# Optimization experiments

Hardware: AMD Instinct MI355X
Metric: run time of the kernel (lower is better)

Reference implementation:

```python
import math
import jax, jax.numpy as jnp
import numpy as np

B, CIN, H, W = 1, 64, 56, 56
MID, HEADS, COUT, MPOS = 32, 8, 64, 56


def setup_inputs() -> dict:
    key = jax.random.key(0)
    ks = jax.random.split(key, 11)
    s = 0.05
    return {
        "x": jax.random.normal(ks[0], (B, CIN, H, W), jnp.float32),
        "Wq": jax.random.normal(ks[1], (MID * HEADS, CIN), jnp.float32) * s,
        "bq": jax.random.normal(ks[2], (MID * HEADS,), jnp.float32) * s,
        "Wk": jax.random.normal(ks[3], (MID * HEADS, CIN), jnp.float32) * s,
        "bk": jax.random.normal(ks[4], (MID * HEADS,), jnp.float32) * s,
        "Wv": jax.random.normal(ks[5], (MID * HEADS, CIN), jnp.float32) * s,
        "bv": jax.random.normal(ks[6], (MID * HEADS,), jnp.float32) * s,
        "Wo": jax.random.normal(ks[7], (COUT, MID * HEADS), jnp.float32) * s,
        "bo": jax.random.normal(ks[8], (COUT,), jnp.float32) * s,
        "row_emb_table": jax.random.normal(ks[9], (2 * MPOS - 1, MID // 2), jnp.float32) * s,
        "col_emb_table": jax.random.normal(ks[10], (2 * MPOS - 1, MID // 2), jnp.float32) * s,
    }


def _conv1x1(x, Wt, bt):
    # 1x1 Conv2d == channel-wise linear
    return jnp.einsum('bcij,dc->bdij', x, Wt) + bt[None, :, None, None]


def reference(x, Wq, bq, Wk, bk, Wv, bv, Wo, bo, row_emb_table, col_emb_table):
    b, cin, h, w = x.shape
    inv = 1.0 / math.sqrt(cin)
    q = _conv1x1(x, Wq, bq).reshape(b, MID, HEADS, h, w)
    k = _conv1x1(x, Wk, bk).reshape(b, MID, HEADS, h, w)
    # relative position indices (constant, derived from arange)
    rel = (jnp.arange(MPOS)[None, :] - jnp.arange(MPOS)[:, None]) + MPOS - 1
    row_emb = row_emb_table[rel[:w, :w].reshape(-1)].T.reshape(MID // 2, w, w)
    col_emb = col_emb_table[rel[:h, :h].reshape(-1)].T.reshape(MID // 2, h, h)
    q_row, q_col = q[:, :MID // 2], q[:, MID // 2:]
    row_scores = jnp.einsum('bchij,cik->bhijk', q_row, row_emb)  # [b,H,h,w,h]
    col_scores = jnp.einsum('bchij,cjl->bhijl', q_col, col_emb)  # [b,H,h,w,w]
    scores = (row_scores[..., :, None] + col_scores[..., None, :]) * inv
    scores = scores + jnp.einsum('bchij,bchkl->bhijkl', q, k) * inv  # [b,H,h,w,h,w]
    probs = jax.nn.softmax(scores.reshape(b, HEADS, h, w, -1), axis=-1).reshape(scores.shape)
    v = _conv1x1(x, Wv, bv).reshape(b, MID, HEADS, h, w)
    o = jnp.einsum('bhijkl,bchkl->bchij', probs, v)
    out = _conv1x1(o.reshape(b, MID * HEADS, h, w), Wo, bo)
    return out
```

## Files before the change

kernel.cpp:

```cpp
#include <hip/hip_runtime.h>

#define HW    3136
#define CIN   64
#define MIDC  32
#define HEADS 8
#define DTOT  256
#define COUTC 64
#define WDIM  56
#define QT    32
#define L2E   1.4426950408889634f

typedef unsigned int uint_t;
typedef _Float16 f16;
typedef __attribute__((ext_vector_type(8))) _Float16 half8;
typedef __attribute__((ext_vector_type(2))) __fp16  fp16x2;
typedef __attribute__((ext_vector_type(4))) float f32x4;
typedef __attribute__((ext_vector_type(2))) float f32x2;

union HU { fp16x2 h; uint_t u; };
__device__ __forceinline__ uint_t pkh(float a, float b) {
    HU u; u.h = __builtin_amdgcn_cvt_pkrtz(a, b); return u.u;
}

__global__ __launch_bounds__(256) void qkv_fused_kernel(
    const float* __restrict__ x,
    const float* __restrict__ Wq, const float* __restrict__ bq,
    const float* __restrict__ Wk, const float* __restrict__ bk,
    const float* __restrict__ Wv, const float* __restrict__ bv,
    const float* __restrict__ Wo,
    f16* __restrict__ qh, f16* __restrict__ kh, f16* __restrict__ vh,
    f16* __restrict__ Wof)
{
    __shared__ float xs[64][36];
    __shared__ float Wlq[64][34];
    __shared__ float Wlk[64][34];
    __shared__ float Wlv[64][34];

    const int tid = threadIdx.x;
    const int h   = blockIdx.y;

    if (blockIdx.x == 98) {
        int r  = blockIdx.y * 8 + (tid >> 5);
        int kp = (tid & 31) * 8;
        half8 v;
        #pragma unroll
        for (int j = 0; j < 8; ++j) {
            int k2 = kp + j;
            int hh = k2 >> 5, mm = k2 & 31;
            v[j] = (f16)Wo[(size_t)r * DTOT + mm * HEADS + hh];
        }
        *(half8*)&Wof[(size_t)r * DTOT + kp] = v;
        return;
    }

    const int P0  = blockIdx.x * 32;

    {   int c = tid >> 2, g = tid & 3;
        const float* src = &x[(size_t)c * HW + P0 + g * 8];
        float4 v0 = *(const float4*)src;
        float4 v1 = *(const float4*)(src + 4);
        *(float4*)&xs[c][g * 8]     = v0;
        *(float4*)&xs[c][g * 8 + 4] = v1;
    }
    {   int m = tid >> 3, c8 = (tid & 7) * 8;
        size_t row = (size_t)(m * HEADS + h) * CIN + c8;
        float4 a0 = *(const float4*)&Wq[row], a1 = *(const float4*)&Wq[row + 4];
        float4 b0 = *(const float4*)&Wk[row], b1 = *(const float4*)&Wk[row + 4];
        float4 c0 = *(const float4*)&Wv[row], c1 = *(const float4*)&Wv[row + 4];
        #pragma unroll
        for (int i = 0; i < 4; ++i) {
            Wlq[c8 + i][m]     = ((const float*)&a0)[i];
            Wlq[c8 + 4 + i][m] = ((const float*)&a1)[i];
            Wlk[c8 + i][m]     = ((const float*)&b0)[i];
            Wlk[c8 + 4 + i][m] = ((const float*)&b1)[i];
            Wlv[c8 + i][m]     = ((const float*)&c0)[i];
            Wlv[c8 + 4 + i][m] = ((const float*)&c1)[i];
        }
    }
    __syncthreads();

    const int a  = tid & 15, pg = tid >> 4;
    const int m0 = a * 2,    p0 = pg * 2;
    const int d0 = m0 * HEADS + h, d1 = d0 + HEADS;

    float q00 = bq[d0], q01 = q00, q10 = bq[d1], q11 = q10;
    float k00 = bk[d0], k01 = k00, k10 = bk[d1], k11 = k10;
    float v00 = bv[d0], v01 = v00, v10 = bv[d1], v11 = v10;

    #pragma unroll 8
    for (int c = 0; c < CIN; ++c) {
        f32x2 xv = *(const f32x2*)&xs[c][p0];
        f32x2 wq = *(const f32x2*)&Wlq[c][m0];
        f32x2 wk = *(const f32x2*)&Wlk[c][m0];
        f32x2 wv = *(const f32x2*)&Wlv[c][m0];
        q00 += wq.x * xv.x; q01 += wq.x * xv.y; q10 += wq.y * xv.x; q11 += wq.y * xv.y;
        k00 += wk.x * xv.x; k01 += wk.x * xv.y; k10 += wk.y * xv.x; k11 += wk.y * xv.y;
        v00 += wv.x * xv.x; v01 += wv.x * xv.y; v10 += wv.y * xv.x; v11 += wv.y * xv.y;
    }

    size_t qk0 = (size_t)h * HW * MIDC + (size_t)(P0 + p0) * MIDC + m0;
    *(uint_t*)&qh[qk0]        = pkh(q00, q10);
    *(uint_t*)&qh[qk0 + MIDC] = pkh(q01, q11);
    *(uint_t*)&kh[qk0]        = pkh(k00, k10);
    *(uint_t*)&kh[qk0 + MIDC] = pkh(k01, k11);
    size_t vb0 = (size_t)(h * MIDC + m0) * HW + P0 + p0;
    *(uint_t*)&vh[vb0]      = pkh(v00, v01);
    *(uint_t*)&vh[vb0 + HW] = pkh(v10, v11);
}

__global__ __launch_bounds__(256, 2) void attn_kernel(
    const f16* __restrict__ qh, const f16* __restrict__ kh,
    const f16* __restrict__ vh,
    const float* __restrict__ rowt, const float* __restrict__ colt,
    f16* __restrict__ obf)
{
    __shared__ f16   Qs[QT][MIDC];
    __shared__ float Rb[QT][57];
    __shared__ float Cb[QT][60];
    __shared__ __align__(16) char pool[18944];
    f16* PlBase = (f16*)pool;

    const int tid   = threadIdx.x;
    const int wave  = tid >> 6, lane = tid & 63;
    const int lin   = blockIdx.y * 98 + blockIdx.x;
    const int h     = lin & 7;
    const int qbase = (lin >> 3) * QT;
    const float c1  = 0.125f * L2E;

    const f16* Qh = qh + (size_t)h * HW * MIDC;
    const f16* Kh = kh + (size_t)h * HW * MIDC;
    const f16* Vh = vh + (size_t)h * MIDC * HW;

    if (tid < 128) {
        int r = tid >> 2, c = (tid & 3) * 8;
        *(uint4*)&Qs[r][c] = *(const uint4*)&Qh[(size_t)(qbase + r) * MIDC + c];
    }
    __syncthreads();

    {
        int q = tid >> 3, sub = tid & 7;
        int qg = qbase + q, qi = qg / WDIM, qj = qg % WDIM;
        half8 qr0 = *(const half8*)&Qs[q][0];
        half8 qr1 = *(const half8*)&Qs[q][8];
        half8 qr2 = *(const half8*)&Qs[q][16];
        half8 qr3 = *(const half8*)&Qs[q][24];
        for (int kp = sub; kp < WDIM; kp += 8) {
            const float* rt = &rowt[(kp - qi + WDIM - 1) * 16];
            const float* ct = &colt[(kp - qj + WDIM - 1) * 16];
            float s = 0.f, s2 = 0.f;
            #pragma unroll
            for (int c = 0; c < 8; ++c) {
                s  += (float)qr0[c] * rt[c] + (float)qr1[c] * rt[8 + c];
                s2 += (float)qr2[c] * ct[c] + (float)qr3[c] * ct[8 + c];
            }
            Rb[q][kp] = s * c1;
            Cb[q][kp] = s2 * c1;
        }
    }
    __syncthreads();

    const int qL  = lane & 15;
    const int grp = lane >> 4;
    half8 qfrag[2];
    qfrag[0] = *(const half8*)&Qs[qL][grp * 8];
    qfrag[1] = *(const half8*)&Qs[16 + qL][grp * 8];

    float lacc[2] = {0.f, 0.f};
    f32x4 o[2][2];
    #pragma unroll
    for (int i = 0; i < 2; ++i) { o[i][0] = (f32x4){0,0,0,0}; o[i][1] = (f32x4){0,0,0,0}; }

    int ki_s[8], kj_s[8];
    #pragma unroll
    for (int s = 0; s < 8; ++s) {
        int key0 = wave * 128 + s * 16 + grp * 4;
        ki_s[s] = key0 / WDIM;
        kj_s[s] = key0 % WDIM;
    }

    f16* Pw = PlBase + wave * (16 * 136);

    for (int j = 0; j < 6; ++j) {
        const int base = 512 * j + 128 * wave;

        half8 kfr[8];
        #pragma unroll
        for (int s = 0; s < 8; ++s)
            kfr[s] = *(const half8*)&Kh[(size_t)(base + s*16 + qL) * MIDC + grp*8];
        half8 vfr[2][4];
        #pragma unroll
        for (int ch = 0; ch < 2; ++ch)
            #pragma unroll
            for (int kf2 = 0; kf2 < 4; ++kf2)
                vfr[ch][kf2] = *(const half8*)
                    &Vh[(size_t)(ch*16 + qL) * HW + base + kf2*32 + grp*8];

        #pragma unroll
        for (int hf = 0; hf < 2; ++hf) {
            const int qrow = hf * 16 + qL;
            f32x4 sc[8];
            __builtin_amdgcn_s_setprio(1);
            #pragma unroll
            for (int s = 0; s < 8; ++s) {
                f32x4 z = {0.f,0.f,0.f,0.f};
                sc[s] = __builtin_amdgcn_mfma_f32_16x16x32_f16(kfr[s], qfrag[hf], z, 0,0,0);
            }
            __builtin_amdgcn_s_setprio(0);
            #pragma unroll
            for (int s = 0; s < 8; ++s) {
                float rb = Rb[qrow][ki_s[s]];
                float4 cbv = *(const float4*)&Cb[qrow][kj_s[s]];
                float e0 = __builtin_amdgcn_exp2f(fmaf(sc[s][0], c1, rb + cbv.x));
                float e1 = __builtin_amdgcn_exp2f(fmaf(sc[s][1], c1, rb + cbv.y));
                float e2 = __builtin_amdgcn_exp2f(fmaf(sc[s][2], c1, rb + cbv.z));
                float e3 = __builtin_amdgcn_exp2f(fmaf(sc[s][3], c1, rb + cbv.w));
                lacc[hf] += (e0 + e1) + (e2 + e3);
                uint2 w2; w2.x = pkh(e0, e1); w2.y = pkh(e2, e3);
                *(uint2*)&Pw[qL * 136 + s * 16 + grp * 4] = w2;
            }
            __builtin_amdgcn_s_setprio(1);
            #pragma unroll
            for (int kf2 = 0; kf2 < 4; ++kf2) {
                half8 pf = *(const half8*)&Pw[qL * 136 + kf2 * 32 + grp * 8];
                o[hf][0] = __builtin_amdgcn_mfma_f32_16x16x32_f16(vfr[0][kf2], pf, o[hf][0], 0,0,0);
                o[hf][1] = __builtin_amdgcn_mfma_f32_16x16x32_f16(vfr[1][kf2], pf, o[hf][1], 0,0,0);
            }
            __builtin_amdgcn_s_setprio(0);
        }

        #pragma unroll
        for (int s = 0; s < 8; ++s) {
            kj_s[s] += 8;
            if (kj_s[s] >= WDIM) { kj_s[s] -= WDIM; ki_s[s] += 10; }
            else                 { ki_s[s] += 9; }
        }
    }

    if (wave < 2) {
        const int base = 3072 + wave * 32;
        half8 kfr[2];
        #pragma unroll
        for (int s = 0; s < 2; ++s)
            kfr[s] = *(const half8*)&Kh[(size_t)(base + s*16 + qL) * MIDC + grp*8];
        half8 vfr2[2];
        #pragma unroll
        for (int ch = 0; ch < 2; ++ch)
            vfr2[ch] = *(const half8*)
                &Vh[(size_t)(ch*16 + qL) * HW + base + grp*8];
        #pragma unroll
        for (int hf = 0; hf < 2; ++hf) {
            const int qrow = hf * 16 + qL;
            f32x4 sc[2];
            #pragma unroll
            for (int s = 0; s < 2; ++s) {
                f32x4 z = {0.f,0.f,0.f,0.f};
                sc[s] = __builtin_amdgcn_mfma_f32_16x16x32_f16(kfr[s], qfrag[hf], z, 0,0,0);
            }
            #pragma unroll
            for (int s = 0; s < 2; ++s) {
                int key0 = base + s * 16 + grp * 4;
                int ki = key0 / WDIM, kj = key0 % WDIM;
                float rb = Rb[qrow][ki];
                float4 cbv = *(const float4*)&Cb[qrow][kj];
                float e0 = __builtin_amdgcn_exp2f(fmaf(sc[s][0], c1, rb + cbv.x));
                float e1 = __builtin_amdgcn_exp2f(fmaf(sc[s][1], c1, rb + cbv.y));
                float e2 = __builtin_amdgcn_exp2f(fmaf(sc[s][2], c1, rb + cbv.z));
                float e3 = __builtin_amdgcn_exp2f(fmaf(sc[s][3], c1, rb + cbv.w));
                lacc[hf] += (e0 + e1) + (e2 + e3);
                uint2 w2; w2.x = pkh(e0, e1); w2.y = pkh(e2, e3);
                *(uint2*)&Pw[qL * 136 + s * 16 + grp * 4] = w2;
            }
            half8 pf = *(const half8*)&Pw[qL * 136 + grp * 8];
            o[hf][0] = __builtin_amdgcn_mfma_f32_16x16x32_f16(vfr2[0], pf, o[hf][0], 0,0,0);
            o[hf][1] = __builtin_amdgcn_mfma_f32_16x16x32_f16(vfr2[1], pf, o[hf][1], 0,0,0);
        }
    }

    #pragma unroll
    for (int hf = 0; hf < 2; ++hf) {
        lacc[hf] += __shfl_xor(lacc[hf], 16);
        lacc[hf] += __shfl_xor(lacc[hf], 32);
    }

    __syncthreads();
    float* MOb = (float*)pool;
    float* Ll  = MOb + 4 * 32 * 36;
    #pragma unroll
    for (int hf = 0; hf < 2; ++hf) {
        int row = wave * 32 + hf * 16 + qL;
        *(f32x4*)&MOb[row * 36 + grp * 4]      = o[hf][0];
        *(f32x4*)&MOb[row * 36 + 16 + grp * 4] = o[hf][1];
        if (grp == 0) Ll[row] = lacc[hf];
    }
    __syncthreads();

    {
        int q = tid & 31, cseg = tid >> 5;
        float l = (Ll[q] + Ll[32+q]) + (Ll[64+q] + Ll[96+q]);
        float invl = 1.f / l;
        int qg = qbase + q;
        float av[4];
        #pragma unroll
        for (int i = 0; i < 4; ++i) {
            int ch = cseg * 4 + i;
            float acc = 0.f;
            #pragma unroll
            for (int w = 0; w < 4; ++w)
                acc += MOb[(w*32 + q) * 36 + ch];
            av[i] = acc * invl;
        }
        uint2 w2; w2.x = pkh(av[0], av[1]); w2.y = pkh(av[2], av[3]);
        *(uint2*)&obf[(size_t)qg * DTOT + h * MIDC + cseg * 4] = w2;
    }
}

__global__ __launch_bounds__(256) void outproj_kernel(
    const f16* __restrict__ obf, const f16* __restrict__ Wof,
    const float* __restrict__ bo, float* __restrict__ out)
{
    const int tid  = threadIdx.x;
    const int mt   = tid >> 6;
    const int lane = tid & 63;
    const int qL = lane & 15, grp = lane >> 4;
    const int p = blockIdx.x * 16 + qL;

    f32x4 acc = (f32x4){0,0,0,0};

    #pragma unroll
    for (int ks = 0; ks < 8; ++ks) {
        half8 bf = *(const half8*)&obf[(size_t)p * DTOT + ks * 32 + grp * 8];
        half8 af = *(const half8*)&Wof[(size_t)(mt * 16 + qL) * DTOT + ks * 32 + grp * 8];
        acc = __builtin_amdgcn_mfma_f32_16x16x32_f16(af, bf, acc, 0, 0, 0);
    }

    #pragma unroll
    for (int r = 0; r < 4; ++r) {
        int d = mt * 16 + grp * 4 + r;
        out[(size_t)d * HW + p] = acc[r] + bo[d];
    }
}

extern "C" void kernel_launch(void* const* d_in, const int* in_sizes, int n_in,
                              void* d_out, int out_size, void* d_ws, size_t ws_size,
                              hipStream_t stream)
{
    const float* x    = (const float*)d_in[0];
    const float* Wq   = (const float*)d_in[1];
    const float* bq   = (const float*)d_in[2];
    const float* Wk   = (const float*)d_in[3];
    const float* bk   = (const float*)d_in[4];
    const float* Wv   = (const float*)d_in[5];
    const float* bv   = (const float*)d_in[6];
    const float* Wo   = (const float*)d_in[7];
    const float* bo   = (const float*)d_in[8];
    const float* rowt = (const float*)d_in[9];
    const float* colt = (const float*)d_in[10];
    float* out = (float*)d_out;

    const size_t N = (size_t)DTOT * HW;
    f16* qh  = (f16*)d_ws;
    f16* kh  = qh + N;
    f16* vh  = kh + N;
    f16* obf = vh + N;
    f16* Wof = obf + N;

    qkv_fused_kernel<<<dim3(99, HEADS), 256, 0, stream>>>(
        x, Wq, bq, Wk, bk, Wv, bv, Wo, qh, kh, vh, Wof);
    attn_kernel<<<dim3(HW / QT, HEADS), 256, 0, stream>>>(qh, kh, vh, rowt, colt, obf);
    outproj_kernel<<<dim3(HW / 16), 256, 0, stream>>>(obf, Wof, bo, out);
}
```

Baseline: 140.3 us.

## Split attention keys across eight waves per block instead of four

The attention kernel now launches 512 threads per block, and each of eight waves handles 64 keys per iteration instead of 128. The tail block is folded into the same lambda body and run by wave 0. Partial outputs are combined in two shared-memory stages and the row sums are reduced over eight waves. This is meant to raise the number of waves in flight for latency hiding. In exchange it adds an extra reduction pass and barrier, and the launch bound of 512 with 2 blocks may limit registers per thread.

```diff
diff --git a/kernel.cpp b/kernel.cpp
--- a/kernel.cpp
+++ b/kernel.cpp
@@ -108,7 +108,7 @@
     *(uint_t*)&vh[vb0 + HW] = pkh(v10, v11);
 }
 
-__global__ __launch_bounds__(256, 2) void attn_kernel(
+__global__ __launch_bounds__(512, 2) void attn_kernel(
     const f16* __restrict__ qh, const f16* __restrict__ kh,
     const f16* __restrict__ vh,
     const float* __restrict__ rowt, const float* __restrict__ colt,
@@ -117,7 +117,7 @@
     __shared__ f16   Qs[QT][MIDC];
     __shared__ float Rb[QT][57];
     __shared__ float Cb[QT][60];
-    __shared__ __align__(16) char pool[18944];
+    __shared__ __align__(16) char pool[19456];
     f16* PlBase = (f16*)pool;
 
     const int tid   = threadIdx.x;
@@ -138,13 +138,13 @@
     __syncthreads();
 
     {
-        int q = tid >> 3, sub = tid & 7;
+        int q = tid >> 4, sub = tid & 15;
         int qg = qbase + q, qi = qg / WDIM, qj = qg % WDIM;
         half8 qr0 = *(const half8*)&Qs[q][0];
         half8 qr1 = *(const half8*)&Qs[q][8];
         half8 qr2 = *(const half8*)&Qs[q][16];
         half8 qr3 = *(const half8*)&Qs[q][24];
-        for (int kp = sub; kp < WDIM; kp += 8) {
+        for (int kp = sub; kp < WDIM; kp += 16) {
             const float* rt = &rowt[(kp - qi + WDIM - 1) * 16];
             const float* ct = &colt[(kp - qj + WDIM - 1) * 16];
             float s = 0.f, s2 = 0.f;
@@ -170,44 +170,42 @@
     #pragma unroll
     for (int i = 0; i < 2; ++i) { o[i][0] = (f32x4){0,0,0,0}; o[i][1] = (f32x4){0,0,0,0}; }
 
-    int ki_s[8], kj_s[8];
-    #pragma unroll
-    for (int s = 0; s < 8; ++s) {
-        int key0 = wave * 128 + s * 16 + grp * 4;
+    int ki_s[4], kj_s[4];
+    #pragma unroll
+    for (int s = 0; s < 4; ++s) {
+        int key0 = wave * 64 + s * 16 + grp * 4;
         ki_s[s] = key0 / WDIM;
         kj_s[s] = key0 % WDIM;
     }
 
-    f16* Pw = PlBase + wave * (16 * 136);
-
-    for (int j = 0; j < 6; ++j) {
-        const int base = 512 * j + 128 * wave;
-
-        half8 kfr[8];
-        #pragma unroll
-        for (int s = 0; s < 8; ++s)
+    f16* Pw = PlBase + wave * (16 * 72);
+
+    auto jbody = [&](const int base) __attribute__((always_inline)) -> void {
+        half8 kfr[4];
+        #pragma unroll
+        for (int s = 0; s < 4; ++s)
             kfr[s] = *(const half8*)&Kh[(size_t)(base + s*16 + qL) * MIDC + grp*8];
-        half8 vfr[2][4];
+        half8 vfr[2][2];
         #pragma unroll
         for (int ch = 0; ch < 2; ++ch)
             #pragma unroll
-            for (int kf2 = 0; kf2 < 4; ++kf2)
+            for (int kf2 = 0; kf2 < 2; ++kf2)
                 vfr[ch][kf2] = *(const half8*)
                     &Vh[(size_t)(ch*16 + qL) * HW + base + kf2*32 + grp*8];
 
         #pragma unroll
         for (int hf = 0; hf < 2; ++hf) {
             const int qrow = hf * 16 + qL;
-            f32x4 sc[8];
+            f32x4 sc[4];
             __builtin_amdgcn_s_setprio(1);
             #pragma unroll
-            for (int s = 0; s < 8; ++s) {
+            for (int s = 0; s < 4; ++s) {
                 f32x4 z = {0.f,0.f,0.f,0.f};
                 sc[s] = __builtin_amdgcn_mfma_f32_16x16x32_f16(kfr[s], qfrag[hf], z, 0,0,0);
             }
             __builtin_amdgcn_s_setprio(0);
             #pragma unroll
-            for (int s = 0; s < 8; ++s) {
+            for (int s = 0; s < 4; ++s) {
                 float rb = Rb[qrow][ki_s[s]];
                 float4 cbv = *(const float4*)&Cb[qrow][kj_s[s]];
                 float e0 = __builtin_amdgcn_exp2f(fmaf(sc[s][0], c1, rb + cbv.x));
@@ -216,12 +214,12 @@
                 float e3 = __builtin_amdgcn_exp2f(fmaf(sc[s][3], c1, rb + cbv.w));
                 lacc[hf] += (e0 + e1) + (e2 + e3);
                 uint2 w2; w2.x = pkh(e0, e1); w2.y = pkh(e2, e3);
-                *(uint2*)&Pw[qL * 136 + s * 16 + grp * 4] = w2;
+                *(uint2*)&Pw[qL * 72 + s * 16 + grp * 4] = w2;
             }
             __builtin_amdgcn_s_setprio(1);
             #pragma unroll
-            for (int kf2 = 0; kf2 < 4; ++kf2) {
-                half8 pf = *(const half8*)&Pw[qL * 136 + kf2 * 32 + grp * 8];
+            for (int kf2 = 0; kf2 < 2; ++kf2) {
+                half8 pf = *(const half8*)&Pw[qL * 72 + kf2 * 32 + grp * 8];
                 o[hf][0] = __builtin_amdgcn_mfma_f32_16x16x32_f16(vfr[0][kf2], pf, o[hf][0], 0,0,0);
                 o[hf][1] = __builtin_amdgcn_mfma_f32_16x16x32_f16(vfr[1][kf2], pf, o[hf][1], 0,0,0);
             }
@@ -229,52 +227,17 @@
         }
 
         #pragma unroll
-        for (int s = 0; s < 8; ++s) {
+        for (int s = 0; s < 4; ++s) {
             kj_s[s] += 8;
             if (kj_s[s] >= WDIM) { kj_s[s] -= WDIM; ki_s[s] += 10; }
             else                 { ki_s[s] += 9; }
         }
-    }
-
-    if (wave < 2) {
-        const int base = 3072 + wave * 32;
-        half8 kfr[2];
-        #pragma unroll
-        for (int s = 0; s < 2; ++s)
-            kfr[s] = *(const half8*)&Kh[(size_t)(base + s*16 + qL) * MIDC + grp*8];
-        half8 vfr2[2];
-        #pragma unroll
-        for (int ch = 0; ch < 2; ++ch)
-            vfr2[ch] = *(const half8*)
-                &Vh[(size_t)(ch*16 + qL) * HW + base + grp*8];
-        #pragma unroll
-        for (int hf = 0; hf < 2; ++hf) {
-            const int qrow = hf * 16 + qL;
-            f32x4 sc[2];
-            #pragma unroll
-            for (int s = 0; s < 2; ++s) {
-                f32x4 z = {0.f,0.f,0.f,0.f};
-                sc[s] = __builtin_amdgcn_mfma_f32_16x16x32_f16(kfr[s], qfrag[hf], z, 0,0,0);
-            }
-            #pragma unroll
-            for (int s = 0; s < 2; ++s) {
-                int key0 = base + s * 16 + grp * 4;
-                int ki = key0 / WDIM, kj = key0 % WDIM;
-                float rb = Rb[qrow][ki];
-                float4 cbv = *(const float4*)&Cb[qrow][kj];
-                float e0 = __builtin_amdgcn_exp2f(fmaf(sc[s][0], c1, rb + cbv.x));
-                float e1 = __builtin_amdgcn_exp2f(fmaf(sc[s][1], c1, rb + cbv.y));
-                float e2 = __builtin_amdgcn_exp2f(fmaf(sc[s][2], c1, rb + cbv.z));
-                float e3 = __builtin_amdgcn_exp2f(fmaf(sc[s][3], c1, rb + cbv.w));
-                lacc[hf] += (e0 + e1) + (e2 + e3);
-                uint2 w2; w2.x = pkh(e0, e1); w2.y = pkh(e2, e3);
-                *(uint2*)&Pw[qL * 136 + s * 16 + grp * 4] = w2;
-            }
-            half8 pf = *(const half8*)&Pw[qL * 136 + grp * 8];
-            o[hf][0] = __builtin_amdgcn_mfma_f32_16x16x32_f16(vfr2[0], pf, o[hf][0], 0,0,0);
-            o[hf][1] = __builtin_amdgcn_mfma_f32_16x16x32_f16(vfr2[1], pf, o[hf][1], 0,0,0);
-        }
-    }
+    };
+
+    for (int j = 0; j < 6; ++j)
+        jbody(512 * j + 64 * wave);
+    if (wave == 0)
+        jbody(3072);
 
     #pragma unroll
     for (int hf = 0; hf < 2; ++hf) {
@@ -284,33 +247,48 @@
 
     __syncthreads();
     float* MOb = (float*)pool;
-    float* Ll  = MOb + 4 * 32 * 36;
+    float* Ll  = (float*)(pool + 18432);
     #pragma unroll
     for (int hf = 0; hf < 2; ++hf) {
-        int row = wave * 32 + hf * 16 + qL;
-        *(f32x4*)&MOb[row * 36 + grp * 4]      = o[hf][0];
-        *(f32x4*)&MOb[row * 36 + 16 + grp * 4] = o[hf][1];
-        if (grp == 0) Ll[row] = lacc[hf];
+        int row = hf * 16 + qL;
+        if (grp == 0) Ll[wave * 32 + row] = lacc[hf];
+        if (wave < 4) {
+            *(f32x4*)&MOb[(wave*32 + row) * 36 + grp * 4]      = o[hf][0];
+            *(f32x4*)&MOb[(wave*32 + row) * 36 + 16 + grp * 4] = o[hf][1];
+        }
+    }
+    __syncthreads();
+    if (wave >= 4) {
+        #pragma unroll
+        for (int hf = 0; hf < 2; ++hf) {
+            int row = (wave - 4) * 32 + hf * 16 + qL;
+            f32x4 a0 = *(f32x4*)&MOb[row * 36 + grp * 4];
+            f32x4 a1 = *(f32x4*)&MOb[row * 36 + 16 + grp * 4];
+            a0 += o[hf][0]; a1 += o[hf][1];
+            *(f32x4*)&MOb[row * 36 + grp * 4]      = a0;
+            *(f32x4*)&MOb[row * 36 + 16 + grp * 4] = a1;
+        }
     }
     __syncthreads();
 
     {
-        int q = tid & 31, cseg = tid >> 5;
-        float l = (Ll[q] + Ll[32+q]) + (Ll[64+q] + Ll[96+q]);
+        int q = tid & 31, cs = tid >> 5;
+        float l = 0.f;
+        #pragma unroll
+        for (int w = 0; w < 8; ++w) l += Ll[w * 32 + q];
         float invl = 1.f / l;
         int qg = qbase + q;
-        float av[4];
-        #pragma unroll
-        for (int i = 0; i < 4; ++i) {
-            int ch = cseg * 4 + i;
+        float av[2];
+        #pragma unroll
+        for (int i = 0; i < 2; ++i) {
+            int ch = cs * 2 + i;
             float acc = 0.f;
             #pragma unroll
             for (int w = 0; w < 4; ++w)
                 acc += MOb[(w*32 + q) * 36 + ch];
             av[i] = acc * invl;
         }
-        uint2 w2; w2.x = pkh(av[0], av[1]); w2.y = pkh(av[2], av[3]);
-        *(uint2*)&obf[(size_t)qg * DTOT + h * MIDC + cseg * 4] = w2;
+        *(uint_t*)&obf[(size_t)qg * DTOT + h * MIDC + cs * 2] = pkh(av[0], av[1]);
     }
 }
 
@@ -366,6 +344,6 @@
 
     qkv_fused_kernel<<<dim3(99, HEADS), 256, 0, stream>>>(
         x, Wq, bq, Wk, bk, Wv, bv, Wo, qh, kh, vh, Wof);
-    attn_kernel<<<dim3(HW / QT, HEADS), 256, 0, stream>>>(qh, kh, vh, rowt, colt, obf);
+    attn_kernel<<<dim3(HW / QT, HEADS), 512, 0, stream>>>(qh, kh, vh, rowt, colt, obf);
     outproj_kernel<<<dim3(HW / 16), 256, 0, stream>>>(obf, Wof, bo, out);
 }
```

After: 146.8 us. +4.7%, slower.
